# Kernel optimization log

Hardware: AMD Instinct MI355X
Metric: run time of the kernel (lower is better)

## Reference

```python
import jax, jax.numpy as jnp
import numpy as np

N, NX, NQ, NU = 262144, 64, 64, 16
STD = 0.5


def setup_inputs() -> dict:
    key = jax.random.key(0)
    ks = jax.random.split(key, 8)
    x = jax.random.normal(ks[0], (N, NX), jnp.float32)
    u = jax.random.normal(ks[1], (N, NU), jnp.float32)
    A = jax.random.normal(ks[2], (NX, NX), jnp.float32) * STD
    B1 = jax.random.normal(ks[3], (NX, NQ), jnp.float32) * STD
    B2 = jax.random.normal(ks[4], (NX, NU), jnp.float32) * STD
    C1 = jax.random.normal(ks[5], (NQ, NX), jnp.float32) * STD
    # D11 is strictly lower triangular (forward substitution / triangular solve)
    D11 = jnp.tril(jax.random.normal(ks[6], (NQ, NQ), jnp.float32) * STD, -1)
    D12 = jax.random.normal(ks[7], (NQ, NU), jnp.float32) * STD
    bv = jnp.zeros((NQ,), jnp.float32)  # bias=False in original module
    bx = jnp.zeros((NX,), jnp.float32)
    return {"x": x, "u": u, "A": A, "B1": B1, "B2": B2,
            "C1": C1, "D11": D11, "D12": D12, "bv": bv, "bx": bx}


def _calculate_w(x, u, C1, D11, D12, bv):
    """Solve w = act(C1 x + D11 w + D12 u + bv) by forward substitution.
    D11 is strictly lower triangular, so row i of w only depends on rows < i."""
    act = jax.nn.relu
    nq = D11.shape[0]
    base = x @ C1.T + u @ D12.T + bv          # (N, nq): input-dependent part
    eye = jnp.eye(nq, dtype=x.dtype)           # one-hot rows for the scatter

    def step(w, inp):
        d_row, b_col, e = inp                  # (nq,), (N,), (nq,)
        v = b_col + w @ d_row                  # (N,)  uses only already-filled w cols
        w = w + act(v)[:, None] * e            # write column i (matches torch select_w)
        return w, None

    w0 = jnp.zeros((x.shape[0], nq), x.dtype)
    w, _ = jax.lax.scan(step, w0, (D11, base.T, eye))
    return w


def reference(x, u, A, B1, B2, C1, D11, D12, bv, bx):
    # x_dot = A x + B1 w + B2 u + bx
    w = _calculate_w(x, u, C1, D11, D12, bv)
    x_dot = x @ A.T + w @ B1.T + u @ B2.T + bx
    return x_dot
```

## Files before the change

### kernel.cpp

```cpp
#include <hip/hip_runtime.h>
#include <utility>

#define NROWS 262144
#define BT 512
#define RPB 256

typedef float f16v __attribute__((ext_vector_type(16)));
typedef float f4v  __attribute__((ext_vector_type(4)));


__global__ void prep_kernel(const float* __restrict__ A, const float* __restrict__ B1,
                            const float* __restrict__ B2, const float* __restrict__ C1,
                            const float* __restrict__ D11, const float* __restrict__ D12,
                            const float* __restrict__ bv, const float* __restrict__ bx,
                            float* __restrict__ ws) {
    int g = blockIdx.x * 256 + threadIdx.x;
    if (g < 4096) {
        int r = g >> 6, c = g & 63;
        int to = c * 64 + r;
        ws[0     + to] = C1[g];
        ws[4096  + to] = D11[g];
        ws[9280  + to] = A[g];
        ws[13376 + to] = B1[g];
    }
    if (g < 1024) {
        int r = g >> 4, c = g & 15;
        int to = c * 64 + r;
        ws[8192  + to] = D12[g];
        ws[17472 + to] = B2[g];
    }
    if (g < 64) {
        ws[9216  + g] = bv[g];
        ws[18496 + g] = bx[g];
    }
}

__device__ __forceinline__ f16v lds16(const float* p) { return *(const f16v*)p; }

__device__ __forceinline__ void fence_sched() { __builtin_amdgcn_sched_barrier(0); }

template<int Q>
__device__ __forceinline__ float qbcast(float v) {
    return __int_as_float(__builtin_amdgcn_update_dpp(
        0, __float_as_int(v), Q * 0x55, 0xF, 0xF, true));
}


template<int I>
__device__ __forceinline__ void substep2(f16v& s0, f16v& s1, const float* D11s,
                                         int c16, int c) {
    const float w0 = fmaxf(qbcast<(I >> 4)>(s0[I & 15]), 0.0f);
    const float w1 = fmaxf(qbcast<(I >> 4)>(s1[I & 15]), 0.0f);
    const f16v m = lds16(D11s + I * 64 + c16);
    s0 += m * w0;
    s1 += m * w1;
    s0[I & 15] = (c == (I >> 4)) ? w0 : s0[I & 15];
    s1[I & 15] = (c == (I >> 4)) ? w1 : s1[I & 15];
}
template<int... Is>
__device__ __forceinline__ void subst_all2(f16v& s0, f16v& s1, const float* D11s,
                                           int c16, int c,
                                           std::integer_sequence<int, Is...>) {
    (substep2<Is>(s0, s1, D11s, c16, c), ...);
}

template<int J>
__device__ __forceinline__ void mv64step2(f16v& a0, f16v& a1, const float* Ms,
                                          int c16, const f16v& f0, const f16v& f1) {
    const f16v m = lds16(Ms + J * 64 + c16);
    a0 += m * qbcast<(J >> 4)>(f0[J & 15]);
    a1 += m * qbcast<(J >> 4)>(f1[J & 15]);
}
template<int... Js>
__device__ __forceinline__ void mv64_2(f16v& a0, f16v& a1, const float* Ms, int c16,
                                       const f16v& f0, const f16v& f1,
                                       std::integer_sequence<int, Js...>) {
    (mv64step2<Js>(a0, a1, Ms, c16, f0, f1), ...);
}

template<int J>
__device__ __forceinline__ void mv16step2(f16v& a0, f16v& a1, const float* Ms,
                                          int c16, const f4v& f0, const f4v& f1) {
    const f16v m = lds16(Ms + J * 64 + c16);
    a0 += m * qbcast<(J >> 2)>(f0[J & 3]);
    a1 += m * qbcast<(J >> 2)>(f1[J & 3]);
}
template<int... Js>
__device__ __forceinline__ void mv16_2(f16v& a0, f16v& a1, const float* Ms, int c16,
                                       const f4v& f0, const f4v& f1,
                                       std::integer_sequence<int, Js...>) {
    (mv16step2<Js>(a0, a1, Ms, c16, f0, f1), ...);
}

__global__ __launch_bounds__(BT, 4) void renl2_fused(const float* __restrict__ x,
                                                     const float* __restrict__ u,
                                                     const float* __restrict__ ws,
                                                     float* __restrict__ out) {
    __shared__ __align__(64) float sm[9280];
    const int tid = threadIdx.x;
    const int c   = tid & 3;
    const int c16 = c << 4;
    const size_t row0 = (size_t)blockIdx.x * RPB;

    const f16v xf0 = *(const f16v*)(x + row0 * 64 + (size_t)tid * 16);
    const f16v xf1 = *(const f16v*)(x + (row0 + 128) * 64 + (size_t)tid * 16);
    const f4v  uf0 = *(const f4v*) (u + row0 * 16 + (size_t)tid * 4);
    const f4v  uf1 = *(const f4v*) (u + (row0 + 128) * 16 + (size_t)tid * 4);

    const float4* wsv = (const float4*)ws;
    float4* smv = (float4*)sm;
#pragma unroll
    for (int i = 0; i < 4; i++) smv[tid + i * BT] = wsv[tid + i * BT];
    if (tid < 2320 - 4 * BT) smv[tid + 4 * BT] = wsv[tid + 4 * BT];
    __syncthreads();

    f16v s0 = lds16(sm + 9216 + c16);
    f16v s1 = s0;
    mv64_2(s0, s1, sm + 0,    c16, xf0, xf1, std::make_integer_sequence<int, 64>{});
    mv16_2(s0, s1, sm + 8192, c16, uf0, uf1, std::make_integer_sequence<int, 16>{});
    fence_sched();

    subst_all2(s0, s1, sm + 4096, c16, c, std::make_integer_sequence<int, 64>{});
    fence_sched();

    __syncthreads();
#pragma unroll
    for (int i = 0; i < 4; i++) smv[tid + i * BT] = wsv[2320 + tid + i * BT];
    if (tid < 2320 - 4 * BT) smv[tid + 4 * BT] = wsv[2320 + tid + 4 * BT];
    __syncthreads();

    f16v acc0 = lds16(sm + 9216 + c16);
    f16v acc1 = acc0;
    mv64_2(acc0, acc1, sm + 4096, c16, s0, s1, std::make_integer_sequence<int, 64>{});
    fence_sched();

    size_t r0 = row0;
    asm volatile("" : "+s"(r0));
    const f16v xg0 = *(const f16v*)(x + r0 * 64 + (size_t)tid * 16);
    const f16v xg1 = *(const f16v*)(x + (r0 + 128) * 64 + (size_t)tid * 16);
    const f4v  ug0 = *(const f4v*) (u + r0 * 16 + (size_t)tid * 4);
    const f4v  ug1 = *(const f4v*) (u + (r0 + 128) * 16 + (size_t)tid * 4);
    mv64_2(acc0, acc1, sm + 0,    c16, xg0, xg1, std::make_integer_sequence<int, 64>{});
    mv16_2(acc0, acc1, sm + 8192, c16, ug0, ug1, std::make_integer_sequence<int, 16>{});

    const size_t q = (size_t)(tid >> 2);
    *(f16v*)(out + (row0 + q) * 64 + c16)       = acc0;
    *(f16v*)(out + (row0 + 128 + q) * 64 + c16) = acc1;
}

extern "C" void kernel_launch(void* const* d_in, const int* in_sizes, int n_in,
                              void* d_out, int out_size, void* d_ws, size_t ws_size,
                              hipStream_t stream) {
    const float* x   = (const float*)d_in[0];
    const float* u   = (const float*)d_in[1];
    const float* A   = (const float*)d_in[2];
    const float* B1  = (const float*)d_in[3];
    const float* B2  = (const float*)d_in[4];
    const float* C1  = (const float*)d_in[5];
    const float* D11 = (const float*)d_in[6];
    const float* D12 = (const float*)d_in[7];
    const float* bv  = (const float*)d_in[8];
    const float* bx  = (const float*)d_in[9];
    float* out = (float*)d_out;
    float* ws  = (float*)d_ws;

    prep_kernel<<<16, 256, 0, stream>>>(A, B1, B2, C1, D11, D12, bv, bx, ws);
    renl2_fused<<<NROWS / RPB, BT, 0, stream>>>(x, u, ws, out);
}
```

Before: 241.4 us.

## Split weight reads between LDS and global/L1, defer relu out of substitution

Matrix-vector loops now read even rows of each weight matrix from LDS and odd rows straight from the global workspace. This halves LDS read bandwidth and routes the rest through the vector cache. The per-step select that wrote the activated value back into s is removed, and one relu over all 16 lanes runs after the substitution. That is valid because later rows only use the relu'd broadcast value. Launch bounds drop to 2 blocks per CU, giving the compiler more registers, at the risk of lower occupancy and extra global load latency.

```diff
diff --git a/kernel.cpp b/kernel.cpp
--- a/kernel.cpp
+++ b/kernel.cpp
@@ -45,67 +45,74 @@
         0, __float_as_int(v), Q * 0x55, 0xF, 0xF, true));
 }
 
-
 template<int I>
-__device__ __forceinline__ void substep2(f16v& s0, f16v& s1, const float* D11s,
-                                         int c16, int c) {
+__device__ __forceinline__ void substep2(f16v& s0, f16v& s1, const float* D11s, int c16) {
     const float w0 = fmaxf(qbcast<(I >> 4)>(s0[I & 15]), 0.0f);
     const float w1 = fmaxf(qbcast<(I >> 4)>(s1[I & 15]), 0.0f);
     const f16v m = lds16(D11s + I * 64 + c16);
     s0 += m * w0;
     s1 += m * w1;
-    s0[I & 15] = (c == (I >> 4)) ? w0 : s0[I & 15];
-    s1[I & 15] = (c == (I >> 4)) ? w1 : s1[I & 15];
 }
 template<int... Is>
 __device__ __forceinline__ void subst_all2(f16v& s0, f16v& s1, const float* D11s,
-                                           int c16, int c,
-                                           std::integer_sequence<int, Is...>) {
-    (substep2<Is>(s0, s1, D11s, c16, c), ...);
+                                           int c16, std::integer_sequence<int, Is...>) {
+    (substep2<Is>(s0, s1, D11s, c16), ...);
+}
+
+__device__ __forceinline__ void relu16(f16v& a) {
+#pragma unroll
+    for (int e = 0; e < 16; e++) a[e] = fmaxf(a[e], 0.0f);
 }
 
 template<int J>
-__device__ __forceinline__ void mv64step2(f16v& a0, f16v& a1, const float* Ms,
-                                          int c16, const f16v& f0, const f16v& f1) {
-    const f16v m = lds16(Ms + J * 64 + c16);
+__device__ __forceinline__ void mv64step2(f16v& a0, f16v& a1, const float* Ml,
+                                          const float* Mg, int c16,
+                                          const f16v& f0, const f16v& f1) {
+    f16v m;
+    if constexpr ((J & 1) == 0) m = lds16(Ml + J * 64 + c16);
+    else                        m = *(const f16v*)(Mg + J * 64 + c16);
     a0 += m * qbcast<(J >> 4)>(f0[J & 15]);
     a1 += m * qbcast<(J >> 4)>(f1[J & 15]);
 }
 template<int... Js>
-__device__ __forceinline__ void mv64_2(f16v& a0, f16v& a1, const float* Ms, int c16,
+__device__ __forceinline__ void mv64_2(f16v& a0, f16v& a1, const float* Ml,
+                                       const float* Mg, int c16,
                                        const f16v& f0, const f16v& f1,
                                        std::integer_sequence<int, Js...>) {
-    (mv64step2<Js>(a0, a1, Ms, c16, f0, f1), ...);
+    (mv64step2<Js>(a0, a1, Ml, Mg, c16, f0, f1), ...);
 }
 
 template<int J>
-__device__ __forceinline__ void mv16step2(f16v& a0, f16v& a1, const float* Ms,
-                                          int c16, const f4v& f0, const f4v& f1) {
-    const f16v m = lds16(Ms + J * 64 + c16);
+__device__ __forceinline__ void mv16step2(f16v& a0, f16v& a1, const float* Ml,
+                                          const float* Mg, int c16,
+                                          const f4v& f0, const f4v& f1) {
+    f16v m;
+    if constexpr ((J & 1) == 0) m = lds16(Ml + J * 64 + c16);
+    else                        m = *(const f16v*)(Mg + J * 64 + c16);
     a0 += m * qbcast<(J >> 2)>(f0[J & 3]);
     a1 += m * qbcast<(J >> 2)>(f1[J & 3]);
 }
 template<int... Js>
-__device__ __forceinline__ void mv16_2(f16v& a0, f16v& a1, const float* Ms, int c16,
+__device__ __forceinline__ void mv16_2(f16v& a0, f16v& a1, const float* Ml,
+                                       const float* Mg, int c16,
                                        const f4v& f0, const f4v& f1,
                                        std::integer_sequence<int, Js...>) {
-    (mv16step2<Js>(a0, a1, Ms, c16, f0, f1), ...);
+    (mv16step2<Js>(a0, a1, Ml, Mg, c16, f0, f1), ...);
 }
 
-__global__ __launch_bounds__(BT, 4) void renl2_fused(const float* __restrict__ x,
+__global__ __launch_bounds__(BT, 2) void renl2_fused(const float* __restrict__ x,
                                                      const float* __restrict__ u,
                                                      const float* __restrict__ ws,
                                                      float* __restrict__ out) {
     __shared__ __align__(64) float sm[9280];
     const int tid = threadIdx.x;
-    const int c   = tid & 3;
-    const int c16 = c << 4;
+    const int c16 = (tid & 3) << 4;
     const size_t row0 = (size_t)blockIdx.x * RPB;
 
     const f16v xf0 = *(const f16v*)(x + row0 * 64 + (size_t)tid * 16);
     const f16v xf1 = *(const f16v*)(x + (row0 + 128) * 64 + (size_t)tid * 16);
-    const f4v  uf0 = *(const f4v*) (u + row0 * 16 + (size_t)tid * 4);
-    const f4v  uf1 = *(const f4v*) (u + (row0 + 128) * 16 + (size_t)tid * 4);
+    const f4v  uf0 = *(const f4v*)(u + row0 * 16 + (size_t)tid * 4);
+    const f4v  uf1 = *(const f4v*)(u + (row0 + 128) * 16 + (size_t)tid * 4);
 
     const float4* wsv = (const float4*)ws;
     float4* smv = (float4*)sm;
@@ -116,11 +123,15 @@
 
     f16v s0 = lds16(sm + 9216 + c16);
     f16v s1 = s0;
-    mv64_2(s0, s1, sm + 0,    c16, xf0, xf1, std::make_integer_sequence<int, 64>{});
-    mv16_2(s0, s1, sm + 8192, c16, uf0, uf1, std::make_integer_sequence<int, 16>{});
+    mv64_2(s0, s1, sm + 0,    ws + 0,    c16, xf0, xf1,
+           std::make_integer_sequence<int, 64>{});
+    mv16_2(s0, s1, sm + 8192, ws + 8192, c16, uf0, uf1,
+           std::make_integer_sequence<int, 16>{});
     fence_sched();
 
-    subst_all2(s0, s1, sm + 4096, c16, c, std::make_integer_sequence<int, 64>{});
+    subst_all2(s0, s1, sm + 4096, c16, std::make_integer_sequence<int, 64>{});
+    relu16(s0);
+    relu16(s1);
     fence_sched();
 
     __syncthreads();
@@ -131,17 +142,20 @@
 
     f16v acc0 = lds16(sm + 9216 + c16);
     f16v acc1 = acc0;
-    mv64_2(acc0, acc1, sm + 4096, c16, s0, s1, std::make_integer_sequence<int, 64>{});
+    mv64_2(acc0, acc1, sm + 4096, ws + 13376, c16, s0, s1,
+           std::make_integer_sequence<int, 64>{});
     fence_sched();
 
     size_t r0 = row0;
     asm volatile("" : "+s"(r0));
     const f16v xg0 = *(const f16v*)(x + r0 * 64 + (size_t)tid * 16);
     const f16v xg1 = *(const f16v*)(x + (r0 + 128) * 64 + (size_t)tid * 16);
-    const f4v  ug0 = *(const f4v*) (u + r0 * 16 + (size_t)tid * 4);
-    const f4v  ug1 = *(const f4v*) (u + (r0 + 128) * 16 + (size_t)tid * 4);
-    mv64_2(acc0, acc1, sm + 0,    c16, xg0, xg1, std::make_integer_sequence<int, 64>{});
-    mv16_2(acc0, acc1, sm + 8192, c16, ug0, ug1, std::make_integer_sequence<int, 16>{});
+    const f4v  ug0 = *(const f4v*)(u + r0 * 16 + (size_t)tid * 4);
+    const f4v  ug1 = *(const f4v*)(u + (r0 + 128) * 16 + (size_t)tid * 4);
+    mv64_2(acc0, acc1, sm + 0,    ws + 9280,  c16, xg0, xg1,
+           std::make_integer_sequence<int, 64>{});
+    mv16_2(acc0, acc1, sm + 8192, ws + 17472, c16, ug0, ug1,
+           std::make_integer_sequence<int, 16>{});
 
     const size_t q = (size_t)(tid >> 2);
     *(f16v*)(out + (row0 + q) * 64 + c16)       = acc0;
```

Measured after the change: 370.4 us. +53.4%, slower.
